# Kernel tuning notes

Measured on AMD Instinct MI355X. Metric: run time of the kernel, lower is better.

Reference implementation:

```python
import jax, jax.numpy as jnp
import numpy as np

K_RATIO = 0.01
SIM_THRESHOLD = 0.6


def _gcn_update(feats, W_gcn, b_gcn):
    # feats: [N, C]. Build edges: inverse_similarity < (1 - thr)/2  <=>  cos sim > thr.
    nf = feats / jnp.maximum(jnp.linalg.norm(feats, axis=1, keepdims=True), 1e-12)
    sim = nf @ nf.T                                  # [N, N]
    inv_sim = (1.0 - sim) * 0.5
    adj = (inv_sim < (1.0 - SIM_THRESHOLD) * 0.5).astype(feats.dtype)  # includes self loops
    deg = jnp.sum(adj, axis=1)
    dinv = jax.lax.rsqrt(jnp.maximum(deg, 1.0))      # D^{-1/2}
    agg = dinv[:, None] * (adj @ (dinv[:, None] * feats))
    return agg @ W_gcn + b_gcn                        # [N, C]


def setup_inputs() -> dict:
    key = jax.random.key(0)
    k1, k2, k3 = jax.random.split(key, 3)
    B, C, H, W = 16, 128, 160, 160
    z = jax.random.normal(k1, (B, C, H, W), dtype=jnp.float32)
    score = jax.random.uniform(k2, (B, H, W), dtype=jnp.float32)
    W_gcn = jax.random.normal(k3, (C, C), dtype=jnp.float32) * (1.0 / np.sqrt(C))
    b_gcn = jnp.zeros((C,), dtype=jnp.float32)
    return {"z": z, "score": score, "W_gcn": W_gcn, "b_gcn": b_gcn}


def reference(z, score, W_gcn, b_gcn):
    B, C, H, W = z.shape
    num_select = int(H * W * K_RATIO)                # 256, static
    flat_score = score.reshape(B, H * W)
    _, top_idx = jax.lax.top_k(flat_score, num_select)   # [B, S]

    flat_z = z.reshape(B, C, H * W)
    idx_bcs = jnp.broadcast_to(top_idx[:, None, :], (B, C, num_select))
    top_features = jnp.take_along_axis(flat_z, idx_bcs, axis=2)  # [B, C, S]
    feats = top_features.transpose(0, 2, 1).reshape(B * num_select, C)  # [N, C]

    updated = _gcn_update(feats, W_gcn, b_gcn)        # [N, C]
    updated = updated.reshape(B, num_select, C).transpose(0, 2, 1)  # [B, C, S]

    b_ix = jnp.arange(B)[:, None, None]
    c_ix = jnp.arange(C)[None, :, None]
    new_flat = flat_z.at[b_ix, c_ix, top_idx[:, None, :]].set(updated)
    return new_flat.reshape(B, C, H, W)
```

## Files before the change

### kernel.cpp

```cpp
#include <hip/hip_runtime.h>
#include <hip/hip_bf16.h>

#define HWs 25600
#define NB 16
#define NC 128
#define NS 256
#define NN 4096
#define N4 13107200
#define CP_U 8
#define K1_CPB 6400

typedef __attribute__((ext_vector_type(8))) short bf16x8;
typedef __attribute__((ext_vector_type(4))) float f32x4;
typedef __attribute__((ext_vector_type(4))) int i32x4;
typedef unsigned long long u64;

template <int U>
__device__ __forceinline__ void copy_slice(const float4* __restrict__ zz,
                                           float4* __restrict__ oo,
                                           int cb, int tid) {
  size_t start = (size_t)cb * (U * 256) + tid;
  float4 v[U];
  #pragma unroll
  for (int k = 0; k < U; ++k) v[k] = zz[start + k * 256];
  __builtin_amdgcn_sched_barrier(0);
  #pragma unroll
  for (int k = 0; k < U; ++k)
    __builtin_nontemporal_store(*(const f32x4*)&v[k], (f32x4*)&oo[start + k * 256]);
}

__global__ __launch_bounds__(256) void k1_kernel(const float* __restrict__ z,
                                                 const float* __restrict__ score,
                                                 float* __restrict__ out,
                                                 int* __restrict__ sel) {
  __shared__ int hist[256];
  __shared__ int scan_s[256];
  __shared__ int scan_eq[256];
  __shared__ int bc_dig, bc_k;
  const int tid = threadIdx.x;
  const int bid = blockIdx.x;

  if (bid >= NB) {
    copy_slice<CP_U>((const float4*)z, (float4*)out, bid - NB, tid);
    return;
  }

  int b = bid;
  const float* sc = score + (size_t)b * HWs;
  const float4* sc4 = (const float4*)sc;

  unsigned prefix = 0; int k = NS;
  for (int d = 3; d >= 0; --d) {
    int sh = d * 8;
    hist[tid] = 0; __syncthreads();
    unsigned maskHigh = (d == 3) ? 0u : (0xFFFFFFFFu << (sh + 8));
    #pragma unroll 5
    for (int i4 = 0; i4 < 25; ++i4) {
      float4 f = sc4[tid * 25 + i4];
      const float* fp = (const float*)&f;
      #pragma unroll
      for (int c = 0; c < 4; ++c) {
        unsigned v = __float_as_uint(fp[c]);
        if ((v & maskHigh) == prefix) atomicAdd(&hist[(v >> sh) & 255], 1);
      }
    }
    __syncthreads();
    int val = hist[255 - tid];
    scan_s[tid] = val; __syncthreads();
    for (int off = 1; off < 256; off <<= 1) {
      int a = (tid >= off) ? scan_s[tid - off] : 0;
      __syncthreads();
      scan_s[tid] += a; __syncthreads();
    }
    int q = 255 - tid;
    int Sq = scan_s[tid];
    int before = Sq - hist[q];
    if (before < k && k <= Sq) { bc_dig = q; bc_k = k - before; }
    __syncthreads();
    prefix |= ((unsigned)bc_dig) << sh;
    k = bc_k;
    __syncthreads();
  }
  unsigned t = prefix;

  int cgt = 0, ceq = 0;
  #pragma unroll 5
  for (int i4 = 0; i4 < 25; ++i4) {
    float4 f = sc4[tid * 25 + i4];
    const float* fp = (const float*)&f;
    #pragma unroll
    for (int c = 0; c < 4; ++c) {
      unsigned v = __float_as_uint(fp[c]);
      cgt += (v > t) ? 1 : 0;
      ceq += (v == t) ? 1 : 0;
    }
  }
  scan_s[tid] = cgt; scan_eq[tid] = ceq; __syncthreads();
  for (int off = 1; off < 256; off <<= 1) {
    int ag = (tid >= off) ? scan_s[tid - off] : 0;
    int ae = (tid >= off) ? scan_eq[tid - off] : 0;
    __syncthreads();
    scan_s[tid] += ag; scan_eq[tid] += ae; __syncthreads();
  }
  int total_gt = scan_s[255];
  int need = NS - total_gt;
  int g = scan_s[tid] - cgt;
  int e = scan_eq[tid] - ceq;
  for (int i4 = 0; i4 < 25; ++i4) {
    float4 f = sc4[tid * 25 + i4];
    const float* fp = (const float*)&f;
    #pragma unroll
    for (int c = 0; c < 4; ++c) {
      int i = tid * 100 + i4 * 4 + c;
      unsigned v = __float_as_uint(fp[c]);
      if (v > t) { sel[b * NS + g] = i; ++g; }
      else if (v == t) { if (e < need) sel[b * NS + total_gt + e] = i; ++e; }
    }
  }
}

__global__ __launch_bounds__(256) void k2_kernel(const float* __restrict__ z,
                                                 const int* __restrict__ sel,
                                                 float* __restrict__ feats,
                                                 ushort* __restrict__ nfb,
                                                 int* __restrict__ deg) {
  const int tid = threadIdx.x;
  const int bid = blockIdx.x;
  if (bid < 4) {
    *(i32x4*)&deg[bid * 1024 + tid * 4] = (i32x4){0, 0, 0, 0};
  }
  int row = bid * 4 + (tid >> 6);
  int lane = tid & 63;
  int b = row >> 8;
  int idx = sel[row];
  const float* zb = z + (size_t)b * NC * HWs + idx;
  float v0 = zb[(size_t)lane * HWs];
  float v1 = zb[(size_t)(lane + 64) * HWs];
  float ss = v0 * v0 + v1 * v1;
  #pragma unroll
  for (int off = 32; off; off >>= 1) ss += __shfl_xor(ss, off);
  float denom = fmaxf(sqrtf(ss), 1e-12f);
  feats[row * NC + lane] = v0;
  feats[row * NC + lane + 64] = v1;
  __hip_bfloat16 h0 = __float2bfloat16(v0 / denom);
  __hip_bfloat16 h1 = __float2bfloat16(v1 / denom);
  nfb[row * NC + lane] = *reinterpret_cast<ushort*>(&h0);
  nfb[row * NC + lane + 64] = *reinterpret_cast<ushort*>(&h1);
}

__global__ __launch_bounds__(256) void k3_kernel(const ushort* __restrict__ nfb,
                                                 u64* __restrict__ adj,
                                                 int* __restrict__ deg) {
  __shared__ __align__(16) ushort tA[64 * 128];
  __shared__ __align__(16) ushort tB[64 * 128];
  __shared__ u64 rowbits[64];
  const int tid = threadIdx.x;
  const int bid = blockIdx.x;
  int I0 = (bid & 63) * 64, J0 = (bid >> 6) * 64;
  if (tid < 64) rowbits[tid] = 0ull;
  for (int f = tid; f < 1024; f += 256) {
    int r = f >> 4, c = f & 15;
    int scnk = c ^ (r & 7);
    *(i32x4*)&tA[r * 128 + scnk * 8] = *(const i32x4*)(nfb + (size_t)(I0 + r) * NC + c * 8);
    *(i32x4*)&tB[r * 128 + scnk * 8] = *(const i32x4*)(nfb + (size_t)(J0 + r) * NC + c * 8);
  }
  __syncthreads();
  int w = tid >> 6, l = tid & 63;
  int r = l & 15, kg = l >> 4;
  f32x4 acc[4] = {{0.f, 0.f, 0.f, 0.f}, {0.f, 0.f, 0.f, 0.f},
                  {0.f, 0.f, 0.f, 0.f}, {0.f, 0.f, 0.f, 0.f}};
  int Ar = 16 * w + r;
  #pragma unroll
  for (int kk = 0; kk < 4; ++kk) {
    int chunkA = (kk * 4 + kg) ^ (Ar & 7);
    bf16x8 a = *(bf16x8*)&tA[Ar * 128 + chunkA * 8];
    #pragma unroll
    for (int j = 0; j < 4; ++j) {
      int Bc = 16 * j + r;
      int chunkB = (kk * 4 + kg) ^ (Bc & 7);
      bf16x8 bf = *(bf16x8*)&tB[Bc * 128 + chunkB * 8];
      acc[j] = __builtin_amdgcn_mfma_f32_16x16x32_bf16(a, bf, acc[j], 0, 0, 0);
    }
  }
  #pragma unroll
  for (int q = 0; q < 4; ++q) {
    u64 m = 0ull;
    #pragma unroll
    for (int j = 0; j < 4; ++j) {
      float simv = acc[j][q];
      if ((1.0f - simv) * 0.5f < 0.2f) m |= 1ull << (16 * j + (l & 15));
    }
    if (m) atomicOr(&rowbits[16 * w + (l >> 4) * 4 + q], m);
  }
  __syncthreads();
  if (tid < 64) {
    u64 rb = rowbits[tid];
    adj[(size_t)(I0 + tid) * 64 + (bid >> 6)] = rb;
    atomicAdd(&deg[I0 + tid], __popcll(rb));
  }
}

__global__ __launch_bounds__(256) void k4_kernel(const u64* __restrict__ adj,
                                                 const float* __restrict__ feats,
                                                 const int* __restrict__ deg,
                                                 const float* __restrict__ Wg,
                                                 const float* __restrict__ bg,
                                                 const int* __restrict__ sel,
                                                 float* __restrict__ out) {
  __shared__ __align__(16) float Wt[NC * 132];
  __shared__ __align__(16) float aggT[16 * 132];
  int tid = threadIdx.x;
  int r0 = blockIdx.x * 16;
  for (int f = tid; f < NC * NC; f += 256) {
    int c = f >> 7, cp = f & 127;
    Wt[cp * 132 + c] = Wg[f];
  }
  int w = tid >> 6, lane = tid & 63;
  for (int rr = 0; rr < 4; ++rr) {
    int lrow = w * 4 + rr;
    int row = r0 + lrow;
    u64 mw = adj[(size_t)row * 64 + lane];
    float dinv_i = 1.0f / sqrtf(fmaxf((float)deg[row], 1.0f));
    float acc0 = 0.f, acc1 = 0.f;
    for (int wi = 0; wi < 64; ++wi) {
      u64 w64 = __shfl((long long)mw, wi);
      while (w64) {
        int bit = __builtin_ctzll(w64);
        w64 &= w64 - 1;
        int j = wi * 64 + bit;
        float dj = 1.0f / sqrtf(fmaxf((float)deg[j], 1.0f));
        acc0 += dj * feats[(size_t)j * NC + lane];
        acc1 += dj * feats[(size_t)j * NC + lane + 64];
      }
    }
    aggT[lrow * 132 + lane] = dinv_i * acc0;
    aggT[lrow * 132 + lane + 64] = dinv_i * acc1;
  }
  __syncthreads();
  int cp = tid & 127;
  int rsub = tid >> 7;
  float acc[8];
  float bb = bg[cp];
  #pragma unroll
  for (int q = 0; q < 8; ++q) acc[q] = bb;
  for (int c4 = 0; c4 < 32; ++c4) {
    float4 w4 = *(const float4*)&Wt[cp * 132 + c4 * 4];
    #pragma unroll
    for (int q = 0; q < 8; ++q) {
      float4 a4 = *(const float4*)&aggT[(rsub + 2 * q) * 132 + c4 * 4];
      acc[q] += a4.x * w4.x + a4.y * w4.y + a4.z * w4.z + a4.w * w4.w;
    }
  }
  #pragma unroll
  for (int q = 0; q < 8; ++q) {
    int row = r0 + rsub + 2 * q;
    int batch = row >> 8;
    int idx = sel[row];
    out[(size_t)(batch * NC + cp) * HWs + idx] = acc[q];
  }
}

extern "C" void kernel_launch(void* const* d_in, const int* in_sizes, int n_in,
                              void* d_out, int out_size, void* d_ws, size_t ws_size,
                              hipStream_t stream) {
  const float* z     = (const float*)d_in[0];
  const float* score = (const float*)d_in[1];
  const float* Wg    = (const float*)d_in[2];
  const float* bg    = (const float*)d_in[3];
  float* out = (float*)d_out;

  char* ws = (char*)d_ws;
  size_t off = 0;
  auto alloc = [&](size_t bytes) {
    void* p = ws + off;
    off = (off + bytes + 255) & ~(size_t)255;
    return p;
  };
  int* sel     = (int*)alloc(NN * sizeof(int));
  float* feats = (float*)alloc((size_t)NN * NC * sizeof(float));
  ushort* nfb  = (ushort*)alloc((size_t)NN * NC * sizeof(ushort));
  u64* adj     = (u64*)alloc((size_t)NN * 64 * sizeof(u64));
  int* deg     = (int*)alloc(NN * sizeof(int));

  k1_kernel<<<NB + K1_CPB, 256, 0, stream>>>(z, score, out, sel);
  k2_kernel<<<NN / 4, 256, 0, stream>>>(z, sel, feats, nfb, deg);
  k3_kernel<<<4096, 256, 0, stream>>>(nfb, adj, deg);
  k4_kernel<<<256, 256, 0, stream>>>(adj, feats, deg, Wg, bg, sel, out);
}
```

Measured before the change: 164.0 us.

## Split bulk copy into hipMemcpyAsync and cache scores in LDS for top-k

The fused kernel that ran the z-to-out copy alongside the per-batch radix top-k is split in two. The copy now goes through hipMemcpyAsync device-to-device, and a separate 16-block top-k kernel loads each batch's scores into shared memory once instead of rereading global memory on every radix pass. This gives up the overlap between the top-k blocks and the copy blocks, since the two now run one after the other on the stream, in return for a presumably faster copy engine or blit path and fewer global reads. The shared-memory loops use scalar strided accesses instead of float4 loads.

Result: slower. 199.4 us (+21.6%).

```diff
diff --git a/kernel.cpp b/kernel.cpp
--- a/kernel.cpp
+++ b/kernel.cpp
@@ -6,67 +6,36 @@
 #define NC 128
 #define NS 256
 #define NN 4096
-#define N4 13107200
-#define CP_U 8
-#define K1_CPB 6400
 
 typedef __attribute__((ext_vector_type(8))) short bf16x8;
 typedef __attribute__((ext_vector_type(4))) float f32x4;
 typedef __attribute__((ext_vector_type(4))) int i32x4;
 typedef unsigned long long u64;
 
-template <int U>
-__device__ __forceinline__ void copy_slice(const float4* __restrict__ zz,
-                                           float4* __restrict__ oo,
-                                           int cb, int tid) {
-  size_t start = (size_t)cb * (U * 256) + tid;
-  float4 v[U];
-  #pragma unroll
-  for (int k = 0; k < U; ++k) v[k] = zz[start + k * 256];
-  __builtin_amdgcn_sched_barrier(0);
-  #pragma unroll
-  for (int k = 0; k < U; ++k)
-    __builtin_nontemporal_store(*(const f32x4*)&v[k], (f32x4*)&oo[start + k * 256]);
-}
-
-__global__ __launch_bounds__(256) void k1_kernel(const float* __restrict__ z,
-                                                 const float* __restrict__ score,
-                                                 float* __restrict__ out,
-                                                 int* __restrict__ sel) {
+__global__ __launch_bounds__(256) void topk_kernel(const float* __restrict__ score,
+                                                   int* __restrict__ sel) {
+  __shared__ unsigned int vals[HWs];
   __shared__ int hist[256];
   __shared__ int scan_s[256];
   __shared__ int scan_eq[256];
   __shared__ int bc_dig, bc_k;
-  const int tid = threadIdx.x;
-  const int bid = blockIdx.x;
-
-  if (bid >= NB) {
-    copy_slice<CP_U>((const float4*)z, (float4*)out, bid - NB, tid);
-    return;
-  }
-
-  int b = bid;
+  int b = blockIdx.x;
+  int tid = threadIdx.x;
   const float* sc = score + (size_t)b * HWs;
-  const float4* sc4 = (const float4*)sc;
-
+  for (int i = tid; i < HWs; i += 256) vals[i] = __float_as_uint(sc[i]);
+  __syncthreads();
   unsigned prefix = 0; int k = NS;
   for (int d = 3; d >= 0; --d) {
     int sh = d * 8;
     hist[tid] = 0; __syncthreads();
     unsigned maskHigh = (d == 3) ? 0u : (0xFFFFFFFFu << (sh + 8));
-    #pragma unroll 5
-    for (int i4 = 0; i4 < 25; ++i4) {
-      float4 f = sc4[tid * 25 + i4];
-      const float* fp = (const float*)&f;
-      #pragma unroll
-      for (int c = 0; c < 4; ++c) {
-        unsigned v = __float_as_uint(fp[c]);
-        if ((v & maskHigh) == prefix) atomicAdd(&hist[(v >> sh) & 255], 1);
-      }
-    }
-    __syncthreads();
-    int val = hist[255 - tid];
-    scan_s[tid] = val; __syncthreads();
+    for (int i = tid; i < HWs; i += 256) {
+      unsigned v = vals[i];
+      if ((v & maskHigh) == prefix) atomicAdd(&hist[(v >> sh) & 255], 1);
+    }
+    __syncthreads();
+    int v = hist[255 - tid];
+    scan_s[tid] = v; __syncthreads();
     for (int off = 1; off < 256; off <<= 1) {
       int a = (tid >= off) ? scan_s[tid - off] : 0;
       __syncthreads();
@@ -82,18 +51,12 @@
     __syncthreads();
   }
   unsigned t = prefix;
-
+  int cstart = tid * 100, cend = cstart + 100;
   int cgt = 0, ceq = 0;
-  #pragma unroll 5
-  for (int i4 = 0; i4 < 25; ++i4) {
-    float4 f = sc4[tid * 25 + i4];
-    const float* fp = (const float*)&f;
-    #pragma unroll
-    for (int c = 0; c < 4; ++c) {
-      unsigned v = __float_as_uint(fp[c]);
-      cgt += (v > t) ? 1 : 0;
-      ceq += (v == t) ? 1 : 0;
-    }
+  for (int i = cstart; i < cend; ++i) {
+    unsigned v = vals[i];
+    cgt += (v > t) ? 1 : 0;
+    ceq += (v == t) ? 1 : 0;
   }
   scan_s[tid] = cgt; scan_eq[tid] = ceq; __syncthreads();
   for (int off = 1; off < 256; off <<= 1) {
@@ -106,16 +69,10 @@
   int need = NS - total_gt;
   int g = scan_s[tid] - cgt;
   int e = scan_eq[tid] - ceq;
-  for (int i4 = 0; i4 < 25; ++i4) {
-    float4 f = sc4[tid * 25 + i4];
-    const float* fp = (const float*)&f;
-    #pragma unroll
-    for (int c = 0; c < 4; ++c) {
-      int i = tid * 100 + i4 * 4 + c;
-      unsigned v = __float_as_uint(fp[c]);
-      if (v > t) { sel[b * NS + g] = i; ++g; }
-      else if (v == t) { if (e < need) sel[b * NS + total_gt + e] = i; ++e; }
-    }
+  for (int i = cstart; i < cend; ++i) {
+    unsigned v = vals[i];
+    if (v > t) { sel[b * NS + g] = i; ++g; }
+    else if (v == t) { if (e < need) sel[b * NS + total_gt + e] = i; ++e; }
   }
 }
 
@@ -282,7 +239,9 @@
   u64* adj     = (u64*)alloc((size_t)NN * 64 * sizeof(u64));
   int* deg     = (int*)alloc(NN * sizeof(int));
 
-  k1_kernel<<<NB + K1_CPB, 256, 0, stream>>>(z, score, out, sel);
+  hipMemcpyAsync(out, z, (size_t)NB * NC * HWs * sizeof(float),
+                 hipMemcpyDeviceToDevice, stream);
+  topk_kernel<<<NB, 256, 0, stream>>>(score, sel);
   k2_kernel<<<NN / 4, 256, 0, stream>>>(z, sel, feats, nfb, deg);
   k3_kernel<<<4096, 256, 0, stream>>>(nfb, adj, deg);
   k4_kernel<<<256, 256, 0, stream>>>(adj, feats, deg, Wg, bg, sel, out);
```
